# Kernel optimization log

Measured on AMD Instinct MI355X. Metric: run time of the kernel, lower is better.

## Reference

```python
import jax, jax.numpy as jnp
import numpy as np

EMBED_DIM = 1024
NUM_HEADS = 16
HEAD_DIM = EMBED_DIM // NUM_HEADS
SEQ_LEN = 4096


def setup_inputs() -> dict:
    key = jax.random.key(0)
    kx, kq, kk, kv = jax.random.split(key, 4)
    x = jax.random.normal(kx, (SEQ_LEN, EMBED_DIM), dtype=jnp.float32)
    Wq = jax.random.normal(kq, (EMBED_DIM, EMBED_DIM), dtype=jnp.float32)
    Wk = jax.random.normal(kk, (EMBED_DIM, EMBED_DIM), dtype=jnp.float32)
    Wv = jax.random.normal(kv, (EMBED_DIM, EMBED_DIM), dtype=jnp.float32)
    return {"x": x, "Wq": Wq, "Wk": Wk, "Wv": Wv}


def reference(x, Wq, Wk, Wv):
    seq_len, embed_dim = x.shape
    h, d = NUM_HEADS, HEAD_DIM
    # project then split heads: [S, E] -> [H, S, D]
    q = (x @ Wq).reshape(seq_len, h, d).transpose(1, 0, 2)
    k = (x @ Wk).reshape(seq_len, h, d).transpose(1, 0, 2)
    v = (x @ Wv).reshape(seq_len, h, d).transpose(1, 0, 2)
    # full [H, S, S] scores, scaled by sqrt(head_dim) (faithful to original)
    scores = jnp.einsum("hsd,htd->hst", q, k) / jnp.sqrt(jnp.asarray(d, dtype=q.dtype))
    weights = jax.nn.softmax(scores, axis=-1)
    out = jnp.einsum("hst,htd->hsd", weights, v)  # [H, S, D]
    return out.transpose(1, 0, 2).reshape(seq_len, embed_dim)
```

## Files before the change

kernel.cpp:

```cpp
#include <hip/hip_runtime.h>
#include <hip/hip_bf16.h>

#define SEQ 4096
#define EMB 1024
#define NHD 16
#define HDD 64

using bf16 = __hip_bfloat16;
using bf16x8 = __attribute__((ext_vector_type(8))) short;
using f32x4  = __attribute__((ext_vector_type(4))) float;

#define MFMA16(a, b, c) __builtin_amdgcn_mfma_f32_16x16x32_bf16((a), (b), (c), 0, 0, 0)

#define QSCALE 0.1803368801111204f

__device__ __forceinline__ float b2f(bf16 b) { return __bfloat162float(b); }

__device__ __forceinline__ void gll16(const void* g, void* l) {
    __builtin_amdgcn_global_load_lds(
        (const __attribute__((address_space(1))) unsigned int*)g,
        (__attribute__((address_space(3))) unsigned int*)l, 16, 0, 0);
}

__global__ void split_kernel(const float* __restrict__ src, bf16* __restrict__ hi,
                             bf16* __restrict__ lo, int n4) {
    int i = blockIdx.x * blockDim.x + threadIdx.x;
    if (i >= n4) return;
    float4 v = ((const float4*)src)[i];
    float vv[4] = {v.x, v.y, v.z, v.w};
#pragma unroll
    for (int j = 0; j < 4; j++) {
        bf16 h = __float2bfloat16(vv[j]);
        hi[i * 4 + j] = h;
        lo[i * 4 + j] = __float2bfloat16(vv[j] - b2f(h));
    }
}

__global__ void wtrans_kernel(const float* __restrict__ Wq, const float* __restrict__ Wk,
                              const float* __restrict__ Wv,
                              bf16* __restrict__ thq, bf16* __restrict__ tlq,
                              bf16* __restrict__ thk, bf16* __restrict__ tlk,
                              bf16* __restrict__ thv, bf16* __restrict__ tlv) {
    __shared__ float tile[32][33];
    const float* W;
    bf16 *wth, *wtl;
    if (blockIdx.z == 0) { W = Wq; wth = thq; wtl = tlq; }
    else if (blockIdx.z == 1) { W = Wk; wth = thk; wtl = tlk; }
    else { W = Wv; wth = thv; wtl = tlv; }
    int n0 = blockIdx.x * 32, k0 = blockIdx.y * 32;
    int tx = threadIdx.x, ty = threadIdx.y;
    for (int r = ty; r < 32; r += 8)
        tile[r][tx] = W[(k0 + r) * EMB + n0 + tx];
    __syncthreads();
    for (int r = ty; r < 32; r += 8) {
        float v = tile[tx][r];
        bf16 h = __float2bfloat16(v);
        wth[(n0 + r) * EMB + k0 + tx] = h;
        wtl[(n0 + r) * EMB + k0 + tx] = __float2bfloat16(v - b2f(h));
    }
}

template <int NTERMS>
__device__ __forceinline__ void proj_loop(
    const bf16* __restrict__ Ah, const bf16* __restrict__ Al,
    const bf16* __restrict__ Bth, const bf16* __restrict__ Btl,
    bf16* lAh, bf16* lAl, bf16* lBh, bf16* lBl,
    int m0, int n0, int t, f32x4 (&acc)[4][4]) {
    const int wid = t >> 6, lane = t & 63, lr = lane & 15, lg = lane >> 4;
    const int wr = (wid >> 1) * 64, wc = (wid & 1) * 64;
    for (int k0 = 0; k0 < EMB; k0 += 32) {
#pragma unroll
        for (int c = t; c < 512; c += 256) {
            int row = c >> 2, slot = c & 3;
            *(uint4*)&lAh[row * 40 + slot * 8] =
                *(const uint4*)&Ah[(m0 + row) * EMB + k0 + slot * 8];
            *(uint4*)&lBh[row * 40 + slot * 8] =
                *(const uint4*)&Bth[(n0 + row) * EMB + k0 + slot * 8];
            if constexpr (NTERMS == 3) {
                *(uint4*)&lAl[row * 40 + slot * 8] =
                    *(const uint4*)&Al[(m0 + row) * EMB + k0 + slot * 8];
                *(uint4*)&lBl[row * 40 + slot * 8] =
                    *(const uint4*)&Btl[(n0 + row) * EMB + k0 + slot * 8];
            }
        }
        __syncthreads();
        bf16x8 fah[4], fbh[4], fal[4], fbl[4];
#pragma unroll
        for (int i = 0; i < 4; i++) {
            fah[i] = *(const bf16x8*)&lAh[(wr + i * 16 + lr) * 40 + lg * 8];
            fbh[i] = *(const bf16x8*)&lBh[(wc + i * 16 + lr) * 40 + lg * 8];
            if constexpr (NTERMS == 3) {
                fal[i] = *(const bf16x8*)&lAl[(wr + i * 16 + lr) * 40 + lg * 8];
                fbl[i] = *(const bf16x8*)&lBl[(wc + i * 16 + lr) * 40 + lg * 8];
            }
        }
#pragma unroll
        for (int i = 0; i < 4; i++)
#pragma unroll
            for (int j = 0; j < 4; j++) {
                acc[i][j] = MFMA16(fah[i], fbh[j], acc[i][j]);
                if constexpr (NTERMS == 3) {
                    acc[i][j] = MFMA16(fah[i], fbl[j], acc[i][j]);
                    acc[i][j] = MFMA16(fal[i], fbh[j], acc[i][j]);
                }
            }
        __syncthreads();
    }
}

__global__ __launch_bounds__(256) void proj_qkv(
    const bf16* __restrict__ xh, const bf16* __restrict__ xl,
    const bf16* __restrict__ thq, const bf16* __restrict__ tlq,
    const bf16* __restrict__ thk, const bf16* __restrict__ tlk,
    const bf16* __restrict__ thv,
    bf16* __restrict__ qh, bf16* __restrict__ ql,
    bf16* __restrict__ kh, bf16* __restrict__ kl, bf16* __restrict__ vt) {
    __shared__ __align__(16) bf16 lAh[128 * 40];
    __shared__ __align__(16) bf16 lAl[128 * 40];
    __shared__ __align__(16) bf16 lBh[128 * 40];
    __shared__ __align__(16) bf16 lBl[128 * 40];
    const int t = threadIdx.x;
    const int m0 = blockIdx.y * 128;
    const int which = blockIdx.x >> 3;
    const int n0 = (blockIdx.x & 7) * 128;

    f32x4 acc[4][4];
#pragma unroll
    for (int i = 0; i < 4; i++)
#pragma unroll
        for (int j = 0; j < 4; j++) acc[i][j] = (f32x4){0.f, 0.f, 0.f, 0.f};

    if (which == 0)
        proj_loop<3>(xh, xl, thq, tlq, lAh, lAl, lBh, lBl, m0, n0, t, acc);
    else if (which == 1)
        proj_loop<3>(xh, xl, thk, tlk, lAh, lAl, lBh, lBl, m0, n0, t, acc);
    else
        proj_loop<1>(xh, xl, thv, nullptr, lAh, lAl, lBh, lBl, m0, n0, t, acc);

    const int wid = t >> 6, lane = t & 63, lr = lane & 15, lg = lane >> 4;
    const int wr = (wid >> 1) * 64, wc = (wid & 1) * 64;

    if (which == 2) {
#pragma unroll
        for (int i = 0; i < 4; i++)
#pragma unroll
            for (int j = 0; j < 4; j++) {
                int n = n0 + wc + j * 16 + lr;
                int m = m0 + wr + i * 16 + lg * 4;
                __hip_bfloat162 p01 = __float22bfloat162_rn(
                    make_float2(acc[i][j][0], acc[i][j][1]));
                __hip_bfloat162 p23 = __float22bfloat162_rn(
                    make_float2(acc[i][j][2], acc[i][j][3]));
                uint2 w;
                w.x = *(unsigned int*)&p01;
                w.y = *(unsigned int*)&p23;
                *(uint2*)&vt[(size_t)n * SEQ + m] = w;
            }
    } else {
        float scale = (which == 0) ? QSCALE : 1.0f;
        bf16* Chi = (which == 0) ? qh : kh;
        bf16* Clo = (which == 0) ? ql : kl;
#pragma unroll
        for (int i = 0; i < 4; i++)
#pragma unroll
            for (int j = 0; j < 4; j++)
#pragma unroll
                for (int q = 0; q < 4; q++) {
                    float cv = acc[i][j][q] * scale;
                    int m = m0 + wr + i * 16 + lg * 4 + q;
                    int n = n0 + wc + j * 16 + lr;
                    bf16 hv = __float2bfloat16(cv);
                    Chi[m * EMB + n] = hv;
                    Clo[m * EMB + n] = __float2bfloat16(cv - b2f(hv));
                }
    }
}

__global__ __launch_bounds__(512, 4) void attn_kernel(
    const bf16* __restrict__ qh, const bf16* __restrict__ ql,
    const bf16* __restrict__ kh, const bf16* __restrict__ kl,
    const bf16* __restrict__ vt, float* __restrict__ out) {
    __shared__ __align__(16) bf16 lKV[2][3][64 * 64];
    __shared__ __align__(16) bf16 lP[8][16 * 64];
    const int t = threadIdx.x;
    const int swz = (blockIdx.x & 7) * 64 + (blockIdx.x >> 3);
    const int h = swz >> 5;
    const int q0 = (swz & 31) * 128;
    const int wid = t >> 6, lane = t & 63, lr = lane & 15, lg = lane >> 4;
    const int wq = wid * 16;

    const bf16* qrh = qh + (size_t)(q0 + wq + lr) * EMB + h * HDD;
    const bf16* qrl = ql + (size_t)(q0 + wq + lr) * EMB + h * HDD;
    bf16x8 fqh[2], fql[2];
#pragma unroll
    for (int hf = 0; hf < 2; hf++) {
        fqh[hf] = *(const bf16x8*)(qrh + hf * 32 + lg * 8);
        fql[hf] = *(const bf16x8*)(qrl + hf * 32 + lg * 8);
    }

    const int srow = lane >> 3, slot = lane & 7;
    const int r = wid * 8 + srow;
    const int sb = (slot ^ (r & 7)) * 16;
    const char* gp[3];
    gp[0] = (const char*)kh + ((size_t)r * EMB + h * HDD) * 2 + sb;
    gp[1] = (const char*)kl + ((size_t)r * EMB + h * HDD) * 2 + sb;
    gp[2] = (const char*)vt + ((size_t)(h * HDD + r) * SEQ) * 2 + sb;
    bf16* lp[3];
#pragma unroll
    for (int i = 0; i < 3; i++) lp[i] = &lKV[0][i][wid * 512];

    f32x4 Ofr[4];
#pragma unroll
    for (int d = 0; d < 4; d++) Ofr[d] = (f32x4){0.f, 0.f, 0.f, 0.f};
    float Mr = -1e30f, Lr = 0.f;

#pragma unroll
    for (int i = 0; i < 3; i++) {
        gll16(gp[i], lp[i]);
        gp[i] += (i < 2) ? (size_t)(64 * EMB * 2) : (size_t)(64 * 2);
    }
    __syncthreads();

    for (int tk = 0; tk < SEQ / 64; tk++) {
        const int cur = tk & 1;
        if (tk < SEQ / 64 - 1) {
#pragma unroll
            for (int i = 0; i < 3; i++) {
                gll16(gp[i], lp[i] + (cur ^ 1) * 12288);
                gp[i] += (i < 2) ? (size_t)(64 * EMB * 2) : (size_t)(64 * 2);
            }
        }
        const char* cKh = (const char*)&lKV[cur][0][0];
        const char* cKl = (const char*)&lKV[cur][1][0];
        const char* cV  = (const char*)&lKV[cur][2][0];

        __builtin_amdgcn_s_setprio(1);
        f32x4 sfr[4];
#pragma unroll
        for (int kc = 0; kc < 4; kc++) {
            int row = kc * 16 + lr;
            const char* rbh = cKh + row * 128;
            const char* rbl = cKl + row * 128;
            f32x4 a = (f32x4){0.f, 0.f, 0.f, 0.f};
#pragma unroll
            for (int hf = 0; hf < 2; hf++) {
                int off = (hf * 64 + lg * 16) ^ ((row & 7) << 4);
                bf16x8 kbh = *(const bf16x8*)(rbh + off);
                bf16x8 kbl = *(const bf16x8*)(rbl + off);
                a = MFMA16(kbh, fqh[hf], a);
                a = MFMA16(kbh, fql[hf], a);
                a = MFMA16(kbl, fqh[hf], a);
            }
            sfr[kc] = a;
        }
        __builtin_amdgcn_s_setprio(0);

        float mx = sfr[0][0];
#pragma unroll
        for (int kc = 0; kc < 4; kc++)
#pragma unroll
            for (int j = 0; j < 4; j++) mx = fmaxf(mx, sfr[kc][j]);
        mx = fmaxf(mx, __shfl_xor(mx, 16));
        mx = fmaxf(mx, __shfl_xor(mx, 32));

        bool resc = !__all(mx <= Mr + 11.5f);
        float mn = resc ? fmaxf(Mr, mx) : Mr;
        float ps = 0.f;
#pragma unroll
        for (int kc = 0; kc < 4; kc++)
#pragma unroll
            for (int j = 0; j < 4; j++) {
                float p = __builtin_exp2f(sfr[kc][j] - mn);
                sfr[kc][j] = p;
                ps += p;
            }
        ps += __shfl_xor(ps, 16);
        ps += __shfl_xor(ps, 32);
        if (resc) {
            float fac = __builtin_exp2f(Mr - mn);
            Mr = mn;
            Lr = Lr * fac + ps;
#pragma unroll
            for (int d = 0; d < 4; d++)
#pragma unroll
                for (int j = 0; j < 4; j++) Ofr[d][j] *= fac;
        } else {
            Lr += ps;
        }

        {
            char* pw = (char*)&lP[wid][0] + lr * 128;
#pragma unroll
            for (int kc = 0; kc < 4; kc++) {
                __hip_bfloat162 p01 =
                    __float22bfloat162_rn(make_float2(sfr[kc][0], sfr[kc][1]));
                __hip_bfloat162 p23 =
                    __float22bfloat162_rn(make_float2(sfr[kc][2], sfr[kc][3]));
                uint2 w;
                w.x = *(unsigned int*)&p01;
                w.y = *(unsigned int*)&p23;
                *(uint2*)(pw + ((kc * 32 + lg * 8) ^ ((lr & 7) << 4))) = w;
            }
        }

        __builtin_amdgcn_s_setprio(1);
#pragma unroll
        for (int ks = 0; ks < 2; ks++) {
            const char* pb = (const char*)&lP[wid][0] + lr * 128 +
                             ((ks * 64 + lg * 16) ^ ((lr & 7) << 4));
            bf16x8 pf = *(const bf16x8*)pb;
#pragma unroll
            for (int df = 0; df < 4; df++) {
                int vrow = df * 16 + lr;
                const char* pv = cV + vrow * 128 +
                                 ((ks * 64 + lg * 16) ^ ((vrow & 7) << 4));
                bf16x8 vf = *(const bf16x8*)pv;
                Ofr[df] = MFMA16(vf, pf, Ofr[df]);
            }
        }
        __builtin_amdgcn_s_setprio(0);

        __syncthreads();
    }

    float inv = 1.0f / Lr;
    float* orow = out + (size_t)(q0 + wq + lr) * EMB + h * HDD;
#pragma unroll
    for (int df = 0; df < 4; df++) {
        float4 o = make_float4(Ofr[df][0] * inv, Ofr[df][1] * inv,
                               Ofr[df][2] * inv, Ofr[df][3] * inv);
        *(float4*)(orow + df * 16 + lg * 4) = o;
    }
}

extern "C" void kernel_launch(void* const* d_in, const int* in_sizes, int n_in,
                              void* d_out, int out_size, void* d_ws, size_t ws_size,
                              hipStream_t stream) {
    const float* x = (const float*)d_in[0];
    const float* Wq = (const float*)d_in[1];
    const float* Wk = (const float*)d_in[2];
    const float* Wv = (const float*)d_in[3];
    float* out = (float*)d_out;

    char* ws = (char*)d_ws;
    size_t off = 0;
    auto alloc = [&](size_t elems) -> bf16* {
        bf16* p = (bf16*)(ws + off);
        off += elems * sizeof(bf16);
        return p;
    };
    bf16* xh = alloc((size_t)SEQ * EMB);
    bf16* xl = alloc((size_t)SEQ * EMB);
    bf16* wthq = alloc((size_t)EMB * EMB);
    bf16* wtlq = alloc((size_t)EMB * EMB);
    bf16* wthk = alloc((size_t)EMB * EMB);
    bf16* wtlk = alloc((size_t)EMB * EMB);
    bf16* wthv = alloc((size_t)EMB * EMB);
    bf16* wtlv = alloc((size_t)EMB * EMB);
    bf16* qh = alloc((size_t)SEQ * EMB);
    bf16* ql = alloc((size_t)SEQ * EMB);
    bf16* kh = alloc((size_t)SEQ * EMB);
    bf16* kl = alloc((size_t)SEQ * EMB);
    bf16* vt = alloc((size_t)SEQ * EMB);
    (void)ws_size; (void)in_sizes; (void)n_in; (void)out_size;

    split_kernel<<<(SEQ * EMB / 4 + 255) / 256, 256, 0, stream>>>(x, xh, xl, SEQ * EMB / 4);
    wtrans_kernel<<<dim3(32, 32, 3), dim3(32, 8), 0, stream>>>(
        Wq, Wk, Wv, wthq, wtlq, wthk, wtlk, wthv, wtlv);
    proj_qkv<<<dim3(24, 32), 256, 0, stream>>>(
        xh, xl, wthq, wtlq, wthk, wtlk, wthv, qh, ql, kh, kl, vt);
    attn_kernel<<<512, 512, 0, stream>>>(qh, ql, kh, kl, vt, out);
}
```

Before: 251.2 us.

## Switch attention to 32x32 MFMA tiles and keep P in registers via permlane swap

The attention kernel now uses 32x32x16 bf16 MFMA, so each wave handles 32 query rows and a block covers 256 queries, which halves the grid to 256 blocks. The softmax probabilities are packed to bf16 and rearranged across lanes with permlane32_swap, so the P tile no longer round-trips through LDS. The goal is fewer LDS reads/writes and K/V reloads per query, plus more efficient MFMA issue. In exchange it uses more registers (launch bounds lowered to 2) and runs only 256 blocks, which may underfill the 256 CUs.

```diff
diff --git a/kernel.cpp b/kernel.cpp
--- a/kernel.cpp
+++ b/kernel.cpp
@@ -9,8 +9,12 @@
 using bf16 = __hip_bfloat16;
 using bf16x8 = __attribute__((ext_vector_type(8))) short;
 using f32x4  = __attribute__((ext_vector_type(4))) float;
+using f32x16 = __attribute__((ext_vector_type(16))) float;
+using u32x4  = __attribute__((ext_vector_type(4))) unsigned int;
+using u32x2  = __attribute__((ext_vector_type(2))) unsigned int;
 
 #define MFMA16(a, b, c) __builtin_amdgcn_mfma_f32_16x16x32_bf16((a), (b), (c), 0, 0, 0)
+#define MFMA32(a, b, c) __builtin_amdgcn_mfma_f32_32x32x16_bf16((a), (b), (c), 0, 0, 0)
 
 #define QSCALE 0.1803368801111204f
 
@@ -20,6 +24,13 @@
     __builtin_amdgcn_global_load_lds(
         (const __attribute__((address_space(1))) unsigned int*)g,
         (__attribute__((address_space(3))) unsigned int*)l, 16, 0, 0);
+}
+
+__device__ __forceinline__ unsigned pack_bf16x2(float a, float b) {
+    __hip_bfloat162 p = __float22bfloat162_rn(make_float2(a, b));
+    unsigned w;
+    __builtin_memcpy(&w, &p, 4);
+    return w;
 }
 
 __global__ void split_kernel(const float* __restrict__ src, bf16* __restrict__ hi,
@@ -147,13 +158,9 @@
             for (int j = 0; j < 4; j++) {
                 int n = n0 + wc + j * 16 + lr;
                 int m = m0 + wr + i * 16 + lg * 4;
-                __hip_bfloat162 p01 = __float22bfloat162_rn(
-                    make_float2(acc[i][j][0], acc[i][j][1]));
-                __hip_bfloat162 p23 = __float22bfloat162_rn(
-                    make_float2(acc[i][j][2], acc[i][j][3]));
                 uint2 w;
-                w.x = *(unsigned int*)&p01;
-                w.y = *(unsigned int*)&p23;
+                w.x = pack_bf16x2(acc[i][j][0], acc[i][j][1]);
+                w.y = pack_bf16x2(acc[i][j][2], acc[i][j][3]);
                 *(uint2*)&vt[(size_t)n * SEQ + m] = w;
             }
     } else {
@@ -176,26 +183,28 @@
     }
 }
 
-__global__ __launch_bounds__(512, 4) void attn_kernel(
+__global__ __launch_bounds__(512, 2) void attn_kernel(
     const bf16* __restrict__ qh, const bf16* __restrict__ ql,
     const bf16* __restrict__ kh, const bf16* __restrict__ kl,
     const bf16* __restrict__ vt, float* __restrict__ out) {
     __shared__ __align__(16) bf16 lKV[2][3][64 * 64];
-    __shared__ __align__(16) bf16 lP[8][16 * 64];
     const int t = threadIdx.x;
-    const int swz = (blockIdx.x & 7) * 64 + (blockIdx.x >> 3);
-    const int h = swz >> 5;
-    const int q0 = (swz & 31) * 128;
-    const int wid = t >> 6, lane = t & 63, lr = lane & 15, lg = lane >> 4;
-    const int wq = wid * 16;
-
-    const bf16* qrh = qh + (size_t)(q0 + wq + lr) * EMB + h * HDD;
-    const bf16* qrl = ql + (size_t)(q0 + wq + lr) * EMB + h * HDD;
-    bf16x8 fqh[2], fql[2];
-#pragma unroll
-    for (int hf = 0; hf < 2; hf++) {
-        fqh[hf] = *(const bf16x8*)(qrh + hf * 32 + lg * 8);
-        fql[hf] = *(const bf16x8*)(qrl + hf * 32 + lg * 8);
+    const int swz = (blockIdx.x & 7) * 32 + (blockIdx.x >> 3);
+    const int h = swz >> 4;
+    const int q0 = (swz & 15) * 256;
+    const int wid = t >> 6, lane = t & 63;
+    const int qq = lane & 31, hi = lane >> 5;
+    const int qrow = q0 + wid * 32 + qq;
+
+    bf16x8 fqh[4], fql[4];
+    {
+        const bf16* qbh = qh + (size_t)qrow * EMB + h * HDD + hi * 8;
+        const bf16* qbl = ql + (size_t)qrow * EMB + h * HDD + hi * 8;
+#pragma unroll
+        for (int ds = 0; ds < 4; ds++) {
+            fqh[ds] = *(const bf16x8*)(qbh + ds * 16);
+            fql[ds] = *(const bf16x8*)(qbl + ds * 16);
+        }
     }
 
     const int srow = lane >> 3, slot = lane & 7;
@@ -209,9 +218,11 @@
 #pragma unroll
     for (int i = 0; i < 3; i++) lp[i] = &lKV[0][i][wid * 512];
 
-    f32x4 Ofr[4];
-#pragma unroll
-    for (int d = 0; d < 4; d++) Ofr[d] = (f32x4){0.f, 0.f, 0.f, 0.f};
+    f32x16 Ofr[2];
+#pragma unroll
+    for (int db = 0; db < 2; db++)
+#pragma unroll
+        for (int rg = 0; rg < 16; rg++) Ofr[db][rg] = 0.f;
     float Mr = -1e30f, Lr = 0.f;
 
 #pragma unroll
@@ -235,87 +246,86 @@
         const char* cV  = (const char*)&lKV[cur][2][0];
 
         __builtin_amdgcn_s_setprio(1);
-        f32x4 sfr[4];
-#pragma unroll
-        for (int kc = 0; kc < 4; kc++) {
-            int row = kc * 16 + lr;
+        f32x16 sfr[2];
+#pragma unroll
+        for (int kb = 0; kb < 2; kb++) {
+            const int row = kb * 32 + qq;
             const char* rbh = cKh + row * 128;
             const char* rbl = cKl + row * 128;
-            f32x4 a = (f32x4){0.f, 0.f, 0.f, 0.f};
-#pragma unroll
-            for (int hf = 0; hf < 2; hf++) {
-                int off = (hf * 64 + lg * 16) ^ ((row & 7) << 4);
-                bf16x8 kbh = *(const bf16x8*)(rbh + off);
-                bf16x8 kbl = *(const bf16x8*)(rbl + off);
-                a = MFMA16(kbh, fqh[hf], a);
-                a = MFMA16(kbh, fql[hf], a);
-                a = MFMA16(kbl, fqh[hf], a);
-            }
-            sfr[kc] = a;
+            const int sw = (row & 7) << 4;
+            f32x16 a;
+#pragma unroll
+            for (int rg = 0; rg < 16; rg++) a[rg] = 0.f;
+#pragma unroll
+            for (int ds = 0; ds < 4; ds++) {
+                const int off = (ds * 32 + hi * 16) ^ sw;
+                bf16x8 kbh_ = *(const bf16x8*)(rbh + off);
+                bf16x8 kbl_ = *(const bf16x8*)(rbl + off);
+                a = MFMA32(kbh_, fqh[ds], a);
+                a = MFMA32(kbh_, fql[ds], a);
+                a = MFMA32(kbl_, fqh[ds], a);
+            }
+            sfr[kb] = a;
         }
         __builtin_amdgcn_s_setprio(0);
 
         float mx = sfr[0][0];
 #pragma unroll
-        for (int kc = 0; kc < 4; kc++)
-#pragma unroll
-            for (int j = 0; j < 4; j++) mx = fmaxf(mx, sfr[kc][j]);
-        mx = fmaxf(mx, __shfl_xor(mx, 16));
+        for (int kb = 0; kb < 2; kb++)
+#pragma unroll
+            for (int rg = 0; rg < 16; rg++) mx = fmaxf(mx, sfr[kb][rg]);
         mx = fmaxf(mx, __shfl_xor(mx, 32));
 
         bool resc = !__all(mx <= Mr + 11.5f);
         float mn = resc ? fmaxf(Mr, mx) : Mr;
         float ps = 0.f;
 #pragma unroll
-        for (int kc = 0; kc < 4; kc++)
-#pragma unroll
-            for (int j = 0; j < 4; j++) {
-                float p = __builtin_exp2f(sfr[kc][j] - mn);
-                sfr[kc][j] = p;
+        for (int kb = 0; kb < 2; kb++)
+#pragma unroll
+            for (int rg = 0; rg < 16; rg++) {
+                float p = __builtin_exp2f(sfr[kb][rg] - mn);
+                sfr[kb][rg] = p;
                 ps += p;
             }
-        ps += __shfl_xor(ps, 16);
         ps += __shfl_xor(ps, 32);
         if (resc) {
             float fac = __builtin_exp2f(Mr - mn);
             Mr = mn;
             Lr = Lr * fac + ps;
 #pragma unroll
-            for (int d = 0; d < 4; d++)
-#pragma unroll
-                for (int j = 0; j < 4; j++) Ofr[d][j] *= fac;
+            for (int db = 0; db < 2; db++)
+#pragma unroll
+                for (int rg = 0; rg < 16; rg++) Ofr[db][rg] *= fac;
         } else {
             Lr += ps;
         }
 
-        {
-            char* pw = (char*)&lP[wid][0] + lr * 128;
-#pragma unroll
-            for (int kc = 0; kc < 4; kc++) {
-                __hip_bfloat162 p01 =
-                    __float22bfloat162_rn(make_float2(sfr[kc][0], sfr[kc][1]));
-                __hip_bfloat162 p23 =
-                    __float22bfloat162_rn(make_float2(sfr[kc][2], sfr[kc][3]));
-                uint2 w;
-                w.x = *(unsigned int*)&p01;
-                w.y = *(unsigned int*)&p23;
-                *(uint2*)(pw + ((kc * 32 + lg * 8) ^ ((lr & 7) << 4))) = w;
-            }
+        bf16x8 pf[4];
+#pragma unroll
+        for (int sl = 0; sl < 4; sl++) {
+            const int kb = sl >> 1, s8 = (sl & 1) * 8;
+            unsigned w01 = pack_bf16x2(sfr[kb][s8 + 0], sfr[kb][s8 + 1]);
+            unsigned w23 = pack_bf16x2(sfr[kb][s8 + 2], sfr[kb][s8 + 3]);
+            unsigned w45 = pack_bf16x2(sfr[kb][s8 + 4], sfr[kb][s8 + 5]);
+            unsigned w67 = pack_bf16x2(sfr[kb][s8 + 6], sfr[kb][s8 + 7]);
+            u32x2 r0 = __builtin_amdgcn_permlane32_swap(w01, w45, false, false);
+            u32x2 r1 = __builtin_amdgcn_permlane32_swap(w23, w67, false, false);
+            u32x4 fw = {r0[0], r1[0], r0[1], r1[1]};
+            bf16x8 pfv;
+            __builtin_memcpy(&pfv, &fw, 16);
+            pf[sl] = pfv;
         }
 
         __builtin_amdgcn_s_setprio(1);
 #pragma unroll
-        for (int ks = 0; ks < 2; ks++) {
-            const char* pb = (const char*)&lP[wid][0] + lr * 128 +
-                             ((ks * 64 + lg * 16) ^ ((lr & 7) << 4));
-            bf16x8 pf = *(const bf16x8*)pb;
-#pragma unroll
-            for (int df = 0; df < 4; df++) {
-                int vrow = df * 16 + lr;
-                const char* pv = cV + vrow * 128 +
-                                 ((ks * 64 + lg * 16) ^ ((vrow & 7) << 4));
+        for (int sl = 0; sl < 4; sl++) {
+#pragma unroll
+            for (int db = 0; db < 2; db++) {
+                const int vd = db * 32 + qq;
+                const char* pv =
+                    cV + vd * 128 + ((sl * 32 + hi * 16) ^ ((vd & 7) << 4));
                 bf16x8 vf = *(const bf16x8*)pv;
-                Ofr[df] = MFMA16(vf, pf, Ofr[df]);
+                Ofr[db] = MFMA32(vf, pf[sl], Ofr[db]);
             }
         }
         __builtin_amdgcn_s_setprio(0);
@@ -324,13 +334,17 @@
     }
 
     float inv = 1.0f / Lr;
-    float* orow = out + (size_t)(q0 + wq + lr) * EMB + h * HDD;
-#pragma unroll
-    for (int df = 0; df < 4; df++) {
-        float4 o = make_float4(Ofr[df][0] * inv, Ofr[df][1] * inv,
-                               Ofr[df][2] * inv, Ofr[df][3] * inv);
-        *(float4*)(orow + df * 16 + lg * 4) = o;
-    }
+    float* orow = out + (size_t)qrow * EMB + h * HDD;
+#pragma unroll
+    for (int db = 0; db < 2; db++)
+#pragma unroll
+        for (int rg = 0; rg < 4; rg++) {
+            float4 o = make_float4(Ofr[db][rg * 4 + 0] * inv,
+                                   Ofr[db][rg * 4 + 1] * inv,
+                                   Ofr[db][rg * 4 + 2] * inv,
+                                   Ofr[db][rg * 4 + 3] * inv);
+            *(float4*)(orow + db * 32 + rg * 8 + hi * 4) = o;
+        }
 }
 
 extern "C" void kernel_launch(void* const* d_in, const int* in_sizes, int n_in,
@@ -369,5 +383,5 @@
         Wq, Wk, Wv, wthq, wtlq, wthk, wtlk, wthv, wtlv);
     proj_qkv<<<dim3(24, 32), 256, 0, stream>>>(
         xh, xl, wthq, wtlq, wthk, wtlk, wthv, qh, ql, kh, kl, vt);
-    attn_kernel<<<512, 512, 0, stream>>>(qh, ql, kh, kl, vt, out);
-}
+    attn_kernel<<<256, 512, 0, stream>>>(qh, ql, kh, kl, vt, out);
+}
```

Result: faster. 243.4 us (-3.1%).
